# Optimization experiments

Hardware: AMD Instinct MI355X
Metric: run time of the kernel (lower is better)

Reference implementation:

```python
import jax, jax.numpy as jnp
import numpy as np

NEG_INF = -1e10  # finite stand-in for torch NEG_INF; safe under logaddexp
EOS = 1
BLANK = -1  # blank is the last vocab index (self.blank = -1)


def setup_inputs() -> dict:
    key = jax.random.key(0)
    k1, k2, k3 = jax.random.split(key, 3)
    T, V = 1500, 32000
    N, U = 8, 10
    ctc_beam = 2048
    ctc_prob = jax.random.normal(k1, (T, V), dtype=jnp.float32)
    g = jax.random.randint(k2, (N, U), 0, V)
    c = jax.random.randint(k3, (N * ctc_beam,), 0, V)
    return {"ctc_prob": ctc_prob, "g": g, "c": c}


def reference(ctc_prob, g, c):
    # --- constructor math ---
    logp = jax.nn.log_softmax(ctc_prob, axis=-1)  # T x V
    T, V = logp.shape
    N, U = g.shape
    NB = c.shape[0]
    ctc_beam = NB // N
    blank_lp = logp[:, BLANK]                     # T
    gamma_b_g0 = jnp.cumsum(blank_lp)             # T  (running blank logprob)
    # state after repeat_interleave(beam) along batch dim -> T x NB
    gamma_b_g = jnp.broadcast_to(gamma_b_g0[:, None], (T, NB))
    gamma_n_g = jnp.full((T, NB), NEG_INF, jnp.float32)
    ctc_score0 = jnp.zeros((NB,), jnp.float32)    # ctc_score repeated to NB

    # --- forward ---
    lp_c = logp[:, c]                             # T x NB, gathered per candidate
    glen = U - 1                                  # static
    start = max(glen, 1)
    if glen == 0:
        init_n = lp_c[0]
    else:
        init_n = jnp.full((NB,), NEG_INF, jnp.float32)
    init_b = jnp.full((NB,), NEG_INF, jnp.float32)
    score0 = init_n
    repeat = jnp.repeat(g[:, -1], ctc_beam) != c  # NB bool
    neg = jnp.float32(NEG_INF)

    def step(carry, xs):
        n_prev, b_prev, score = carry
        gb_gm1, gn_gm1, lp_c_t, lp_b_t = xs
        term = jnp.where(repeat, gn_gm1, neg)
        phi = jnp.logaddexp(gb_gm1, term)
        n_t = jnp.logaddexp(n_prev, phi) + lp_c_t
        b_t = jnp.logaddexp(b_prev, n_prev) + lp_b_t
        score = jnp.logaddexp(score, phi + lp_c_t)
        return (n_t, b_t, score), None

    xs = (
        gamma_b_g[start - 1:T - 1],                               # gamma_b_g[t-1]
        gamma_n_g[start - 1:T - 1],                               # gamma_n_g[t-1]
        lp_c[start:],                                             # ctc_prob[t, c]
        jnp.broadcast_to(blank_lp[start:, None], (T - start, NB)),  # ctc_prob[t, blank]
    )
    (_, _, score), _ = jax.lax.scan(step, (init_n, init_b, score0), xs)

    is_eos = c == EOS
    gamma_nb_g = jnp.logaddexp(gamma_b_g[-1], gamma_n_g[-1])
    score = jnp.where(is_eos, gamma_nb_g, score)
    delta_score = (score - ctc_score0).reshape(-1, ctc_beam)  # N x ctc_beam
    return delta_score
```

## Files before the change

kernel.cpp:

```cpp
#include <hip/hip_runtime.h>
#include <hip/hip_fp16.h>

#define T_DIM   1500
#define V4      8000
#define START_T 9
#define NB      16384
#define BLOCK   512
#define CPT     32
#define NPAIR   16
#define NJ      16
#define TAIL_N  320
#define ROWS    6
#define NCHUNK  250
#define NEGBIG  -3.0e38f
#define EOS_ID  1
#define LN2     0.69314718055994531f
#define L2E     1.44269504088896341f

#if __has_builtin(__builtin_amdgcn_exp2f)
__device__ __forceinline__ float fexp2(float x) { return __builtin_amdgcn_exp2f(x); }
#else
__device__ __forceinline__ float fexp2(float x) { return __expf(x * LN2); }
#endif
#if __has_builtin(__builtin_amdgcn_logf)
__device__ __forceinline__ float flog2(float x) { return __builtin_amdgcn_logf(x); }
#else
__device__ __forceinline__ float flog2(float x) { return __logf(x) * L2E; }
#endif

#define WG_BARRIER() do { \
  asm volatile("s_waitcnt lgkmcnt(0)" ::: "memory"); \
  __builtin_amdgcn_s_barrier(); \
  asm volatile("" ::: "memory"); \
} while (0)

struct alignas(8) H4 { __half2 a, b; };

__global__ __launch_bounds__(BLOCK, 2)
void ctc_k1(const float* __restrict__ P, const int* __restrict__ cidx,
            float* __restrict__ Lws, float* __restrict__ Sblank)
{
  __shared__ __align__(16) __half rowh[2][32768];
  __shared__ float red[2][12];
  const int tid = threadIdx.x;
  const int q   = blockIdx.x;
  const int t0  = q * ROWS;

  unsigned cidp[NPAIR];
  float s[CPT];
#pragma unroll
  for (int j = 0; j < NPAIR; ++j) {
    unsigned c0 = (unsigned)cidx[(2*j  )*BLOCK + tid] * 2u;
    unsigned c1 = (unsigned)cidx[(2*j+1)*BLOCK + tid] * 2u;
    cidp[j] = c0 | (c1 << 16);
    s[2*j] = 0.f; s[2*j+1] = 0.f;
  }

  const float4* __restrict__ P4 = (const float4*)P;
  const bool tailv = (tid < TAIL_N);

  float4 va[NJ], vb[NJ];

  auto LOAD = [&](float4 (&v)[NJ], int t) {
    const float4* rp = P4 + (long)t * V4;
#pragma unroll
    for (int j = 0; j < 15; ++j) v[j] = rp[j*BLOCK + tid];
    v[15] = tailv ? rp[15*BLOCK + tid] : make_float4(NEGBIG, NEGBIG, NEGBIG, NEGBIG);
  };

  auto STAGE = [&](float4 (&v)[NJ], int buf) {
    float ls = 0.f;
    H4* rw = (H4*)rowh[buf];
#pragma unroll
    for (int j = 0; j < NJ; ++j) {
      float p0 = fexp2(v[j].x * L2E);
      float p1 = fexp2(v[j].y * L2E);
      float p2 = fexp2(v[j].z * L2E);
      float p3 = fexp2(v[j].w * L2E);
      ls += (p0 + p1) + (p2 + p3);
      H4 h; h.a = __floats2half2_rn(p0, p1); h.b = __floats2half2_rn(p2, p3);
      rw[j*BLOCK + tid] = h;
    }
#pragma unroll
    for (int d = 1; d < 64; d <<= 1) ls += __shfl_xor(ls, d);
    if ((tid & 63) == 0) red[buf][tid >> 6] = ls;
    if (tid == TAIL_N - 1) red[buf][8] = v[15].w * L2E;
  };

  float Blocal2 = 0.f;
  auto GATHER = [&](int t, int buf) {
    float sum = red[buf][0];
#pragma unroll
    for (int w = 1; w < 8; ++w) sum += red[buf][w];
    const float lse2 = flog2(sum);
    if (t >= START_T) {
      const float sc = fexp2(Blocal2 - lse2);
      const char* rb = (const char*)rowh[buf];
#pragma unroll
      for (int j = 0; j < NPAIR; ++j) {
        unsigned pk = cidp[j];
        float p0 = __half2float(*(const __half*)(rb + (pk & 0xffffu)));
        float p1 = __half2float(*(const __half*)(rb + (pk >> 16)));
        s[2*j]   = fmaf(sc, p0, s[2*j]);
        s[2*j+1] = fmaf(sc, p1, s[2*j+1]);
      }
    }
    Blocal2 += red[buf][8] - lse2;
  };

  LOAD(va, t0 + 0);
  LOAD(vb, t0 + 1);
  STAGE(va, 0);
  WG_BARRIER();

  LOAD(va, t0 + 2);  GATHER(t0 + 0, 0);  STAGE(vb, 1);  WG_BARRIER();
  LOAD(vb, t0 + 3);  GATHER(t0 + 1, 1);  STAGE(va, 0);  WG_BARRIER();
  LOAD(va, t0 + 4);  GATHER(t0 + 2, 0);  STAGE(vb, 1);  WG_BARRIER();
  LOAD(vb, t0 + 5);  GATHER(t0 + 3, 1);  STAGE(va, 0);  WG_BARRIER();
                     GATHER(t0 + 4, 0);  STAGE(vb, 1);  WG_BARRIER();
                     GATHER(t0 + 5, 1);

#pragma unroll
  for (int k = 0; k < CPT; ++k) {
    float L = (s[k] > 0.f) ? flog2(s[k]) * LN2 : NEGBIG;
    Lws[(long)q*NB + k*BLOCK + tid] = L;
  }
  if (tid == 0) Sblank[q] = Blocal2 * LN2;
}

#define K3_BLOCK 256
#define K3_CPB   128

__global__ __launch_bounds__(K3_BLOCK)
void ctc_k3(const float* __restrict__ Lws, const float* __restrict__ Sblank,
            const int* __restrict__ cidx, float* __restrict__ out, int nchunk)
{
  __shared__ float base[258];
  __shared__ float wsum[4];
  __shared__ float redm[K3_BLOCK], reds[K3_BLOCK];
  const int tid = threadIdx.x;

  float orig = (tid < nchunk) ? Sblank[tid] : 0.f;
  float x = orig;
#pragma unroll
  for (int d = 1; d < 64; d <<= 1) {
    float y = __shfl_up(x, d);
    if ((tid & 63) >= d) x += y;
  }
  if ((tid & 63) == 63) wsum[tid >> 6] = x;
  __syncthreads();
  {
    const int w = tid >> 6;
    float pre = 0.f;
    if (w > 0) pre += wsum[0];
    if (w > 1) pre += wsum[1];
    if (w > 2) pre += wsum[2];
    x += pre;
  }
  if (tid < nchunk)      base[tid] = x - orig;
  if (tid == nchunk - 1) base[nchunk] = x;
  __syncthreads();

  const int half = tid >> 7;
  const int cl   = tid & 127;
  const int i    = blockIdx.x * K3_CPB + cl;
  const int hl   = (nchunk + 1) >> 1;
  const int c0   = half * hl;
  int c1 = c0 + hl; if (c1 > nchunk) c1 = nchunk;

  float mm = NEGBIG, ss = 0.f;
#pragma unroll 4
  for (int q2 = c0; q2 < c1; ++q2) {
    float L = Lws[(long)q2*NB + i] + base[q2];
    float nm = fmaxf(mm, L);
    ss = ss*__expf(mm - nm) + __expf(L - nm);
    mm = nm;
  }
  redm[tid] = mm; reds[tid] = ss;
  __syncthreads();
  if (half == 0) {
    float om = redm[tid + 128], os = reds[tid + 128];
    float nm = fmaxf(mm, om);
    ss = ss*__expf(mm - nm) + os*__expf(om - nm);
    mm = nm;
    float sc = mm + __logf(ss);
    out[i] = (cidx[i] == EOS_ID) ? base[nchunk] : sc;
  }
}

extern "C" void kernel_launch(void* const* d_in, const int* in_sizes, int n_in,
                              void* d_out, int out_size, void* d_ws, size_t ws_size,
                              hipStream_t stream)
{
  const float* P    = (const float*)d_in[0];
  const int*   cidx = (const int*)d_in[2];
  float*       out  = (float*)d_out;

  float* Lws    = (float*)d_ws;
  float* Sblank = Lws + (long)NCHUNK * NB;

  ctc_k1<<<dim3(NCHUNK), dim3(BLOCK), 0, stream>>>(P, cidx, Lws, Sblank);
  ctc_k3<<<dim3(NB / K3_CPB), dim3(K3_BLOCK), 0, stream>>>(Lws, Sblank, cidx, out, NCHUNK);
}
```

Measured before the change: 54.67 us.

## Stream rows via async global-to-LDS loads and widen the k3 chunk split

The row load in k1 no longer goes through large float4 register arrays. Each row is now streamed in 4KB slices with global_load_lds into a double-buffered LDS staging area, using explicit vmcnt waits, and then exponentiated into an fp16 row buffer. This is meant to cut register pressure and keep loads in flight while the exp and stage work runs, at the cost of more LDS use (about 160KB per block, which may limit occupancy) and finer-grained synchronisation. k3 now splits the 250 chunks four ways per column instead of two, launching 256 blocks for more parallelism in the logsumexp reduction.

After: 56.04 us. +2.5%, slower.

```diff
diff --git a/kernel.cpp b/kernel.cpp
--- a/kernel.cpp
+++ b/kernel.cpp
@@ -2,14 +2,13 @@
 #include <hip/hip_fp16.h>
 
 #define T_DIM   1500
-#define V4      8000
+#define ROW_F   32000
+#define TOT_F   48000000L
 #define START_T 9
 #define NB      16384
 #define BLOCK   512
 #define CPT     32
 #define NPAIR   16
-#define NJ      16
-#define TAIL_N  320
 #define ROWS    6
 #define NCHUNK  250
 #define NEGBIG  -3.0e38f
@@ -34,102 +33,118 @@
   asm volatile("" ::: "memory"); \
 } while (0)
 
-struct alignas(8) H4 { __half2 a, b; };
+typedef __attribute__((address_space(1))) void* as1_ptr;
+typedef __attribute__((address_space(3))) void* as3_ptr;
 
 __global__ __launch_bounds__(BLOCK, 2)
 void ctc_k1(const float* __restrict__ P, const int* __restrict__ cidx,
             float* __restrict__ Lws, float* __restrict__ Sblank)
 {
-  __shared__ __align__(16) __half rowh[2][32768];
+  __shared__ __align__(16) __half Ah[64000];
+  __shared__ __align__(16) float  Bs[2][4096];
   __shared__ float red[2][12];
   const int tid = threadIdx.x;
+  const int w   = tid >> 6;
+  const int l   = tid & 63;
   const int q   = blockIdx.x;
   const int t0  = q * ROWS;
 
   unsigned cidp[NPAIR];
-  float s[CPT];
+  float acc[CPT];
 #pragma unroll
   for (int j = 0; j < NPAIR; ++j) {
     unsigned c0 = (unsigned)cidx[(2*j  )*BLOCK + tid] * 2u;
     unsigned c1 = (unsigned)cidx[(2*j+1)*BLOCK + tid] * 2u;
     cidp[j] = c0 | (c1 << 16);
-    s[2*j] = 0.f; s[2*j+1] = 0.f;
-  }
-
-  const float4* __restrict__ P4 = (const float4*)P;
-  const bool tailv = (tid < TAIL_N);
-
-  float4 va[NJ], vb[NJ];
-
-  auto LOAD = [&](float4 (&v)[NJ], int t) {
-    const float4* rp = P4 + (long)t * V4;
-#pragma unroll
-    for (int j = 0; j < 15; ++j) v[j] = rp[j*BLOCK + tid];
-    v[15] = tailv ? rp[15*BLOCK + tid] : make_float4(NEGBIG, NEGBIG, NEGBIG, NEGBIG);
+    acc[2*j] = 0.f; acc[2*j+1] = 0.f;
+  }
+
+  float blankv  = 0.f;
+  float Blocal2 = 0.f;
+
+  auto ISSUE = [&](int g) {
+    const int rr = g >> 3, ss = g & 7;
+    long f0 = (long)(t0 + rr) * ROW_F + (ss << 12) + (w << 9) + (l << 2);
+    long f1 = f0 + 256;
+    f0 = (f0 > TOT_F - 4) ? (TOT_F - 4) : f0;
+    f1 = (f1 > TOT_F - 4) ? (TOT_F - 4) : f1;
+    float* b0 = &Bs[g & 1][(w << 9)];
+    __builtin_amdgcn_global_load_lds((as1_ptr)(P + f0), (as3_ptr)(b0      ), 16, 0, 0);
+    __builtin_amdgcn_global_load_lds((as1_ptr)(P + f1), (as3_ptr)(b0 + 256), 16, 0, 0);
   };
 
-  auto STAGE = [&](float4 (&v)[NJ], int buf) {
-    float ls = 0.f;
-    H4* rw = (H4*)rowh[buf];
-#pragma unroll
-    for (int j = 0; j < NJ; ++j) {
-      float p0 = fexp2(v[j].x * L2E);
-      float p1 = fexp2(v[j].y * L2E);
-      float p2 = fexp2(v[j].z * L2E);
-      float p3 = fexp2(v[j].w * L2E);
-      ls += (p0 + p1) + (p2 + p3);
-      H4 h; h.a = __floats2half2_rn(p0, p1); h.b = __floats2half2_rn(p2, p3);
-      rw[j*BLOCK + tid] = h;
+  auto STAGE_ROW = [&](int gbase, int nb, bool LASTROW) {
+    float psum = 0.f;
+#pragma unroll
+    for (int ss = 0; ss < 8; ++ss) {
+      const int g = gbase + ss;
+      if (LASTROW && ss == 7) { asm volatile("s_waitcnt vmcnt(0)" ::: "memory"); }
+      else                    { asm volatile("s_waitcnt vmcnt(2)" ::: "memory"); }
+      const int len = (ss == 7) ? 3328 : 4096;
+      const int rem = len - (w << 9);
+      const int nj  = (rem >= 512) ? 8 : (rem > 0 ? (rem >> 6) : 0);
+      float x[8];
+      const float* Bsl = &Bs[g & 1][(w << 9) + l];
+#pragma unroll
+      for (int j = 0; j < 8; ++j) if (j < nj) x[j] = Bsl[j << 6];
+      asm volatile("s_waitcnt lgkmcnt(0)" ::: "memory");
+      if (g + 2 < 48) ISSUE(g + 2);
+      __half* Adst = Ah + nb * ROW_F + (ss << 12) + (w << 9) + l;
+#pragma unroll
+      for (int j = 0; j < 8; ++j) if (j < nj) {
+        float px = fexp2(x[j] * L2E);
+        psum += px;
+        Adst[j << 6] = __float2half_rn(px);
+        if (ss == 7 && j == 3 && tid == 447) blankv = x[j];
+      }
     }
 #pragma unroll
-    for (int d = 1; d < 64; d <<= 1) ls += __shfl_xor(ls, d);
-    if ((tid & 63) == 0) red[buf][tid >> 6] = ls;
-    if (tid == TAIL_N - 1) red[buf][8] = v[15].w * L2E;
+    for (int d = 1; d < 64; d <<= 1) psum += __shfl_xor(psum, d);
+    if (l == 0) red[nb][w] = psum;
+    if (tid == 447) red[nb][8] = blankv * L2E;
   };
 
-  float Blocal2 = 0.f;
-  auto GATHER = [&](int t, int buf) {
-    float sum = red[buf][0];
-#pragma unroll
-    for (int w = 1; w < 8; ++w) sum += red[buf][w];
+  auto GATHER = [&](int r) {
+    const int b = r & 1;
+    float sum = red[b][0];
+#pragma unroll
+    for (int ww = 1; ww < 8; ++ww) sum += red[b][ww];
     const float lse2 = flog2(sum);
-    if (t >= START_T) {
+    if (t0 + r >= START_T) {
       const float sc = fexp2(Blocal2 - lse2);
-      const char* rb = (const char*)rowh[buf];
+      const char* rb = (const char*)Ah + b * 64000;
 #pragma unroll
       for (int j = 0; j < NPAIR; ++j) {
         unsigned pk = cidp[j];
         float p0 = __half2float(*(const __half*)(rb + (pk & 0xffffu)));
         float p1 = __half2float(*(const __half*)(rb + (pk >> 16)));
-        s[2*j]   = fmaf(sc, p0, s[2*j]);
-        s[2*j+1] = fmaf(sc, p1, s[2*j+1]);
+        acc[2*j]   = fmaf(sc, p0, acc[2*j]);
+        acc[2*j+1] = fmaf(sc, p1, acc[2*j+1]);
       }
     }
-    Blocal2 += red[buf][8] - lse2;
+    Blocal2 += red[b][8] - lse2;
   };
 
-  LOAD(va, t0 + 0);
-  LOAD(vb, t0 + 1);
-  STAGE(va, 0);
+  ISSUE(0); ISSUE(1);
+  STAGE_ROW(0, 0, false);
   WG_BARRIER();
 
-  LOAD(va, t0 + 2);  GATHER(t0 + 0, 0);  STAGE(vb, 1);  WG_BARRIER();
-  LOAD(vb, t0 + 3);  GATHER(t0 + 1, 1);  STAGE(va, 0);  WG_BARRIER();
-  LOAD(va, t0 + 4);  GATHER(t0 + 2, 0);  STAGE(vb, 1);  WG_BARRIER();
-  LOAD(vb, t0 + 5);  GATHER(t0 + 3, 1);  STAGE(va, 0);  WG_BARRIER();
-                     GATHER(t0 + 4, 0);  STAGE(vb, 1);  WG_BARRIER();
-                     GATHER(t0 + 5, 1);
+  for (int r = 0; r < 5; ++r) {
+    GATHER(r);
+    STAGE_ROW((r + 1) * 8, (r + 1) & 1, r == 4);
+    WG_BARRIER();
+  }
+  GATHER(5);
 
 #pragma unroll
   for (int k = 0; k < CPT; ++k) {
-    float L = (s[k] > 0.f) ? flog2(s[k]) * LN2 : NEGBIG;
+    float L = (acc[k] > 0.f) ? flog2(acc[k]) * LN2 : NEGBIG;
     Lws[(long)q*NB + k*BLOCK + tid] = L;
   }
   if (tid == 0) Sblank[q] = Blocal2 * LN2;
 }
 
 #define K3_BLOCK 256
-#define K3_CPB   128
 
 __global__ __launch_bounds__(K3_BLOCK)
 void ctc_k3(const float* __restrict__ Lws, const float* __restrict__ Sblank,
@@ -137,7 +152,7 @@
 {
   __shared__ float base[258];
   __shared__ float wsum[4];
-  __shared__ float redm[K3_BLOCK], reds[K3_BLOCK];
+  __shared__ float pm[4][64], pv[4][64];
   const int tid = threadIdx.x;
 
   float orig = (tid < nchunk) ? Sblank[tid] : 0.f;
@@ -150,40 +165,42 @@
   if ((tid & 63) == 63) wsum[tid >> 6] = x;
   __syncthreads();
   {
-    const int w = tid >> 6;
+    const int ww = tid >> 6;
     float pre = 0.f;
-    if (w > 0) pre += wsum[0];
-    if (w > 1) pre += wsum[1];
-    if (w > 2) pre += wsum[2];
+    if (ww > 0) pre += wsum[0];
+    if (ww > 1) pre += wsum[1];
+    if (ww > 2) pre += wsum[2];
     x += pre;
   }
   if (tid < nchunk)      base[tid] = x - orig;
   if (tid == nchunk - 1) base[nchunk] = x;
   __syncthreads();
 
-  const int half = tid >> 7;
-  const int cl   = tid & 127;
-  const int i    = blockIdx.x * K3_CPB + cl;
-  const int hl   = (nchunk + 1) >> 1;
-  const int c0   = half * hl;
-  int c1 = c0 + hl; if (c1 > nchunk) c1 = nchunk;
-
-  float mm = NEGBIG, ss = 0.f;
-#pragma unroll 4
+  const int c = tid & 63;
+  const int p = tid >> 6;
+  const int i = blockIdx.x * 64 + c;
+  const int c0 = p * 63;
+  int c1 = c0 + 63; if (c1 > nchunk) c1 = nchunk;
+
+  float mm = NEGBIG, ssum = 0.f;
+#pragma unroll 8
   for (int q2 = c0; q2 < c1; ++q2) {
     float L = Lws[(long)q2*NB + i] + base[q2];
     float nm = fmaxf(mm, L);
-    ss = ss*__expf(mm - nm) + __expf(L - nm);
+    ssum = ssum*__expf(mm - nm) + __expf(L - nm);
     mm = nm;
   }
-  redm[tid] = mm; reds[tid] = ss;
+  pm[p][c] = mm; pv[p][c] = ssum;
   __syncthreads();
-  if (half == 0) {
-    float om = redm[tid + 128], os = reds[tid + 128];
-    float nm = fmaxf(mm, om);
-    ss = ss*__expf(mm - nm) + os*__expf(om - nm);
-    mm = nm;
-    float sc = mm + __logf(ss);
+  if (p == 0) {
+#pragma unroll
+    for (int pp = 1; pp < 4; ++pp) {
+      float om = pm[pp][c], os = pv[pp][c];
+      float nm = fmaxf(mm, om);
+      ssum = ssum*__expf(mm - nm) + os*__expf(om - nm);
+      mm = nm;
+    }
+    float sc = mm + __logf(ssum);
     out[i] = (cidx[i] == EOS_ID) ? base[nchunk] : sc;
   }
 }
@@ -200,5 +217,5 @@
   float* Sblank = Lws + (long)NCHUNK * NB;
 
   ctc_k1<<<dim3(NCHUNK), dim3(BLOCK), 0, stream>>>(P, cidx, Lws, Sblank);
-  ctc_k3<<<dim3(NB / K3_CPB), dim3(K3_BLOCK), 0, stream>>>(Lws, Sblank, cidx, out, NCHUNK);
+  ctc_k3<<<dim3(NB / 64), dim3(K3_BLOCK), 0, stream>>>(Lws, Sblank, cidx, out, NCHUNK);
 }
```

## Split row staging into halves with single LDS buffer and smaller chunks

Applied to the files above, without the earlier changes.

The row-staging kernel now loads and exponentiates each vocabulary row in two halves into one shared fp16 buffer, instead of double-buffering full rows. Rows per block drop from 6 to 3, doubling the grid to 500 blocks. The aim is to cut register and LDS footprint so more blocks are resident and the load imbalance across CUs shrinks. In exchange each row now needs two barriers, and the per-chunk workspace doubles, so the reduction kernel, reworked to 8 partitions of 64 candidates, must read twice as much data.

Result: slower. 66.64 us (+21.9%).

```diff
diff --git a/kernel.cpp b/kernel.cpp
--- a/kernel.cpp
+++ b/kernel.cpp
@@ -2,16 +2,18 @@
 #include <hip/hip_fp16.h>
 
 #define T_DIM   1500
+#define ROW_F   32000
 #define V4      8000
+#define HALF_F4 4000
 #define START_T 9
 #define NB      16384
 #define BLOCK   512
 #define CPT     32
 #define NPAIR   16
-#define NJ      16
-#define TAIL_N  320
-#define ROWS    6
-#define NCHUNK  250
+#define NJH     8
+#define TAILH   416
+#define ROWS    3
+#define NCHUNK  500
 #define NEGBIG  -3.0e38f
 #define EOS_ID  1
 #define LN2     0.69314718055994531f
@@ -40,8 +42,8 @@
 void ctc_k1(const float* __restrict__ P, const int* __restrict__ cidx,
             float* __restrict__ Lws, float* __restrict__ Sblank)
 {
-  __shared__ __align__(16) __half rowh[2][32768];
-  __shared__ float red[2][12];
+  __shared__ __align__(16) __half A[ROW_F];
+  __shared__ float red[12];
   const int tid = threadIdx.x;
   const int q   = blockIdx.x;
   const int t0  = q * ROWS;
@@ -57,45 +59,44 @@
   }
 
   const float4* __restrict__ P4 = (const float4*)P;
-  const bool tailv = (tid < TAIL_N);
-
-  float4 va[NJ], vb[NJ];
-
-  auto LOAD = [&](float4 (&v)[NJ], int t) {
-    const float4* rp = P4 + (long)t * V4;
-#pragma unroll
-    for (int j = 0; j < 15; ++j) v[j] = rp[j*BLOCK + tid];
-    v[15] = tailv ? rp[15*BLOCK + tid] : make_float4(NEGBIG, NEGBIG, NEGBIG, NEGBIG);
+  const bool tailv = (tid < TAILH);
+
+  float4 va[NJH];
+  float  psum   = 0.f;
+  float  blankv = 0.f;
+
+  auto LOADH = [&](int t, int h) {
+    const float4* rp = P4 + (long)t * V4 + h * HALF_F4;
+#pragma unroll
+    for (int j = 0; j < 7; ++j) va[j] = rp[j*BLOCK + tid];
+    if (tailv) va[7] = rp[7*BLOCK + tid];
   };
 
-  auto STAGE = [&](float4 (&v)[NJ], int buf) {
-    float ls = 0.f;
-    H4* rw = (H4*)rowh[buf];
-#pragma unroll
-    for (int j = 0; j < NJ; ++j) {
-      float p0 = fexp2(v[j].x * L2E);
-      float p1 = fexp2(v[j].y * L2E);
-      float p2 = fexp2(v[j].z * L2E);
-      float p3 = fexp2(v[j].w * L2E);
-      ls += (p0 + p1) + (p2 + p3);
-      H4 h; h.a = __floats2half2_rn(p0, p1); h.b = __floats2half2_rn(p2, p3);
-      rw[j*BLOCK + tid] = h;
+  auto STAGEH = [&](int h) {
+    H4* rw = (H4*)A + h * HALF_F4;
+#pragma unroll
+    for (int j = 0; j < NJH; ++j) {
+      if (j == 7 && !tailv) break;
+      float p0 = fexp2(va[j].x * L2E);
+      float p1 = fexp2(va[j].y * L2E);
+      float p2 = fexp2(va[j].z * L2E);
+      float p3 = fexp2(va[j].w * L2E);
+      psum += (p0 + p1) + (p2 + p3);
+      H4 hh; hh.a = __floats2half2_rn(p0, p1); hh.b = __floats2half2_rn(p2, p3);
+      rw[j*BLOCK + tid] = hh;
+      if (h == 1 && j == 7 && tid == TAILH - 1) blankv = va[7].w * L2E;
     }
-#pragma unroll
-    for (int d = 1; d < 64; d <<= 1) ls += __shfl_xor(ls, d);
-    if ((tid & 63) == 0) red[buf][tid >> 6] = ls;
-    if (tid == TAIL_N - 1) red[buf][8] = v[15].w * L2E;
   };
 
   float Blocal2 = 0.f;
-  auto GATHER = [&](int t, int buf) {
-    float sum = red[buf][0];
-#pragma unroll
-    for (int w = 1; w < 8; ++w) sum += red[buf][w];
+  auto GATHER = [&](int t) {
+    float sum = red[0];
+#pragma unroll
+    for (int w = 1; w < 8; ++w) sum += red[w];
     const float lse2 = flog2(sum);
     if (t >= START_T) {
       const float sc = fexp2(Blocal2 - lse2);
-      const char* rb = (const char*)rowh[buf];
+      const char* rb = (const char*)A;
 #pragma unroll
       for (int j = 0; j < NPAIR; ++j) {
         unsigned pk = cidp[j];
@@ -105,20 +106,27 @@
         s[2*j+1] = fmaf(sc, p1, s[2*j+1]);
       }
     }
-    Blocal2 += red[buf][8] - lse2;
+    Blocal2 += red[8] - lse2;
   };
 
-  LOAD(va, t0 + 0);
-  LOAD(vb, t0 + 1);
-  STAGE(va, 0);
-  WG_BARRIER();
-
-  LOAD(va, t0 + 2);  GATHER(t0 + 0, 0);  STAGE(vb, 1);  WG_BARRIER();
-  LOAD(vb, t0 + 3);  GATHER(t0 + 1, 1);  STAGE(va, 0);  WG_BARRIER();
-  LOAD(va, t0 + 4);  GATHER(t0 + 2, 0);  STAGE(vb, 1);  WG_BARRIER();
-  LOAD(vb, t0 + 5);  GATHER(t0 + 3, 1);  STAGE(va, 0);  WG_BARRIER();
-                     GATHER(t0 + 4, 0);  STAGE(vb, 1);  WG_BARRIER();
-                     GATHER(t0 + 5, 1);
+  LOADH(t0, 0);
+
+  for (int r = 0; r < ROWS; ++r) {
+    const int t = t0 + r;
+    psum = 0.f;
+    STAGEH(0);
+    LOADH(t, 1);
+    STAGEH(1);
+    if (r + 1 < ROWS) LOADH(t + 1, 0);
+    float ls = psum;
+#pragma unroll
+    for (int d = 1; d < 64; d <<= 1) ls += __shfl_xor(ls, d);
+    if ((tid & 63) == 0) red[tid >> 6] = ls;
+    if (tid == TAILH - 1) red[8] = blankv;
+    WG_BARRIER();
+    GATHER(t);
+    WG_BARRIER();
+  }
 
 #pragma unroll
   for (int k = 0; k < CPT; ++k) {
@@ -128,16 +136,15 @@
   if (tid == 0) Sblank[q] = Blocal2 * LN2;
 }
 
-#define K3_BLOCK 256
-#define K3_CPB   128
+#define K3_BLOCK 512
 
 __global__ __launch_bounds__(K3_BLOCK)
 void ctc_k3(const float* __restrict__ Lws, const float* __restrict__ Sblank,
             const int* __restrict__ cidx, float* __restrict__ out, int nchunk)
 {
-  __shared__ float base[258];
-  __shared__ float wsum[4];
-  __shared__ float redm[K3_BLOCK], reds[K3_BLOCK];
+  __shared__ float base[K3_BLOCK + 1];
+  __shared__ float wsum[8];
+  __shared__ float pm[8][64], pv[8][64];
   const int tid = threadIdx.x;
 
   float orig = (tid < nchunk) ? Sblank[tid] : 0.f;
@@ -152,37 +159,35 @@
   {
     const int w = tid >> 6;
     float pre = 0.f;
-    if (w > 0) pre += wsum[0];
-    if (w > 1) pre += wsum[1];
-    if (w > 2) pre += wsum[2];
+    for (int k = 0; k < w; ++k) pre += wsum[k];
     x += pre;
   }
-  if (tid < nchunk)      base[tid] = x - orig;
-  if (tid == nchunk - 1) base[nchunk] = x;
+  base[tid] = x - orig;
   __syncthreads();
 
-  const int half = tid >> 7;
-  const int cl   = tid & 127;
-  const int i    = blockIdx.x * K3_CPB + cl;
-  const int hl   = (nchunk + 1) >> 1;
-  const int c0   = half * hl;
-  int c1 = c0 + hl; if (c1 > nchunk) c1 = nchunk;
+  const int c = tid & 63;
+  const int p = tid >> 6;
+  const int i = blockIdx.x * 64 + c;
+  const int c0 = p * 63;
+  int c1 = c0 + 63; if (c1 > nchunk) c1 = nchunk;
 
   float mm = NEGBIG, ss = 0.f;
-#pragma unroll 4
   for (int q2 = c0; q2 < c1; ++q2) {
     float L = Lws[(long)q2*NB + i] + base[q2];
     float nm = fmaxf(mm, L);
     ss = ss*__expf(mm - nm) + __expf(L - nm);
     mm = nm;
   }
-  redm[tid] = mm; reds[tid] = ss;
+  pm[p][c] = mm; pv[p][c] = ss;
   __syncthreads();
-  if (half == 0) {
-    float om = redm[tid + 128], os = reds[tid + 128];
-    float nm = fmaxf(mm, om);
-    ss = ss*__expf(mm - nm) + os*__expf(om - nm);
-    mm = nm;
+  if (p == 0) {
+#pragma unroll
+    for (int pp = 1; pp < 8; ++pp) {
+      float om = pm[pp][c], os = pv[pp][c];
+      float nm = fmaxf(mm, om);
+      ss = ss*__expf(mm - nm) + os*__expf(om - nm);
+      mm = nm;
+    }
     float sc = mm + __logf(ss);
     out[i] = (cidx[i] == EOS_ID) ? base[nchunk] : sc;
   }
@@ -200,5 +205,5 @@
   float* Sblank = Lws + (long)NCHUNK * NB;
 
   ctc_k1<<<dim3(NCHUNK), dim3(BLOCK), 0, stream>>>(P, cidx, Lws, Sblank);
-  ctc_k3<<<dim3(NB / K3_CPB), dim3(K3_BLOCK), 0, stream>>>(Lws, Sblank, cidx, out, NCHUNK);
+  ctc_k3<<<dim3(NB / 64), dim3(K3_BLOCK), 0, stream>>>(Lws, Sblank, cidx, out, NCHUNK);
 }
```
